# Performance work log

Hardware: AMD Instinct MI355X
Metric: run time of the kernel (lower is better)

Reference implementation:

```python
import jax, jax.numpy as jnp
import numpy as np

WEIGHT_BIT = 8
BIAS_BIT = 32
EPS = 1e-8


def setup_inputs() -> dict:
    key = jax.random.key(0)
    k1, k2, k3, k4 = jax.random.split(key, 4)
    N, IN, OUT = 65536, 512, 512
    # x_q: already-quantized int8-range activations stored as float32
    x_q = jax.random.randint(k1, (N, IN), -128, 128).astype(jnp.float32)
    weight = jax.random.normal(k2, (OUT, IN), dtype=jnp.float32) * 0.05
    bias = jax.random.normal(k3, (OUT,), dtype=jnp.float32) * 0.01
    scale_x = jax.random.uniform(k4, (1,), dtype=jnp.float32, minval=0.01, maxval=0.1)
    return {"x_q": x_q, "weight": weight, "bias": bias, "scale_x": scale_x}


def _symmetric_quant_weight(w, bit):
    # per-output-channel symmetric quantization (min/max over dim=1)
    n = float(2 ** (bit - 1) - 1)  # 127 for 8-bit
    sat = jnp.maximum(jnp.abs(w.min(axis=1)), jnp.abs(w.max(axis=1)))  # [OUT]
    scale = jnp.maximum(sat, EPS) / n                                   # [OUT]
    w_q = jnp.clip(jnp.round(w / scale[:, None]), -n - 1.0, n)
    return w_q, scale


def reference(x_q, weight, bias, scale_x):
    w_q, scale_w = _symmetric_quant_weight(weight, WEIGHT_BIT)
    scale_out = scale_w * scale_x[0]          # [OUT] per-channel output scale
    nb = float(2 ** (BIAS_BIT - 1) - 1)
    b_q = jnp.clip(jnp.round(bias / scale_out), -nb - 1.0, nb)
    # integer-only matmul: int32 GEMM with int32 bias
    out_q = (jnp.dot(x_q.astype(jnp.int32), w_q.astype(jnp.int32).T)
             + b_q.astype(jnp.int32)[None, :])
    return out_q, scale_out.reshape(1, -1)
```

## Files before the change

### kernel.cpp

```cpp
#include <hip/hip_runtime.h>
#include <hip/hip_bf16.h>

typedef __attribute__((ext_vector_type(8))) short bf16x8;
typedef __attribute__((ext_vector_type(4))) float f32x4;

#define KDIM 512
#define NDIM 512
#define BM 128
#define BN 64
#define BK 32
#define NT (KDIM / BK)

__device__ __forceinline__ unsigned int pack_bf16(float a, float b) {
  return (__builtin_bit_cast(unsigned int, a) >> 16) |
         (__builtin_bit_cast(unsigned int, b) & 0xffff0000u);
}

__global__ __launch_bounds__(64)
void quant_w_kernel(const float* __restrict__ W, const float* __restrict__ bias,
                    const float* __restrict__ scale_x,
                    ushort* __restrict__ Wq_arr, float* __restrict__ bq,
                    float* __restrict__ so_out) {
  const int n = blockIdx.x;
  const int l = threadIdx.x;
  const float* row = W + (size_t)n * KDIM;
  float4 v0 = *(const float4*)(row + l * 8);
  float4 v1 = *(const float4*)(row + l * 8 + 4);
  float m = fmaxf(fmaxf(fmaxf(fabsf(v0.x), fabsf(v0.y)), fmaxf(fabsf(v0.z), fabsf(v0.w))),
                  fmaxf(fmaxf(fabsf(v1.x), fabsf(v1.y)), fmaxf(fabsf(v1.z), fabsf(v1.w))));
#pragma unroll
  for (int off = 32; off; off >>= 1) m = fmaxf(m, __shfl_xor(m, off, 64));
  const float scale = fmaxf(m, 1e-8f) / 127.0f;
  float vals[8] = {v0.x, v0.y, v0.z, v0.w, v1.x, v1.y, v1.z, v1.w};
  unsigned int packed[4];
#pragma unroll
  for (int i = 0; i < 4; ++i) {
    float qa = fminf(fmaxf(rintf(vals[2 * i] / scale), -128.f), 127.f);
    float qb = fminf(fmaxf(rintf(vals[2 * i + 1] / scale), -128.f), 127.f);
    packed[i] = pack_bf16(qa, qb);
  }
  const size_t slot = ((size_t)(n >> 4) * 16 + (l >> 2)) * 64 + (n & 15) + (l & 3) * 16;
  *(uint4*)(Wq_arr + slot * 8) = make_uint4(packed[0], packed[1], packed[2], packed[3]);
  if (l == 0) {
    float so = scale * scale_x[0];
    so_out[n] = so;
    bq[n] = rintf(bias[n] / so);
  }
}

__global__ __launch_bounds__(256, 5)
void gemm_kernel(const float* __restrict__ X, const ushort* __restrict__ Wqa,
                 const float* __restrict__ bq, float* __restrict__ Out) {
  __shared__ __align__(16) float As[2][BM * BK];

  const int nblk = gridDim.x;
  int swz = blockIdx.x;
  if ((nblk & 7) == 0)
    swz = (blockIdx.x & 7) * (nblk >> 3) + (blockIdx.x >> 3);
  const int bm = swz >> 3;
  const int bn = swz & 7;

  const int tid = threadIdx.x;
  const int l = tid & 63, w = tid >> 6;
  const int lr = l & 15, lk = l >> 4;

  const float* xbase = X + (size_t)bm * BM * KDIM;
  const ushort* bbase = Wqa + (((size_t)bn * 4 * 16) * 64 + l) * 8;

  f32x4 acc[2][4];
#pragma unroll
  for (int i = 0; i < 2; ++i)
#pragma unroll
    for (int j = 0; j < 4; ++j) acc[i][j] = (f32x4){0.f, 0.f, 0.f, 0.f};

  auto stage = [&](int t, int buf) {
#pragma unroll
    for (int i = 0; i < 4; ++i) {
      int s = i * 256 + tid;
      int row = s >> 3;
      int c = s & 7;
      int sc = c ^ (row & 7);
      const float* g = xbase + (size_t)row * KDIM + t * BK + sc * 4;
      float* lp = &As[buf][0] + (size_t)s * 4;
      __builtin_amdgcn_global_load_lds(
          (const __attribute__((address_space(1))) unsigned int*)g,
          (__attribute__((address_space(3))) unsigned int*)lp, 16, 0, 0);
    }
  };

  auto compute = [&](int t, int buf) {
    const char* pA = (const char*)&As[buf][0];
    bf16x8 bf[4];
#pragma unroll
    for (int nf = 0; nf < 4; ++nf)
      bf[nf] = *(const bf16x8*)(bbase + ((size_t)nf * 16 + t) * 512);
    bf16x8 af[2];
#pragma unroll
    for (int mf = 0; mf < 2; ++mf) {
      int r = w * 32 + mf * 16 + lr;
      int swzr = (r & 7) << 4;
      float4 lo = *(const float4*)(pA + (r * 128 + (((lk * 2) << 4) ^ swzr)));
      float4 hi = *(const float4*)(pA + (r * 128 + (((lk * 2 + 1) << 4) ^ swzr)));
      union { unsigned int u[4]; bf16x8 v; } rr;
      rr.u[0] = pack_bf16(lo.x, lo.y);
      rr.u[1] = pack_bf16(lo.z, lo.w);
      rr.u[2] = pack_bf16(hi.x, hi.y);
      rr.u[3] = pack_bf16(hi.z, hi.w);
      af[mf] = rr.v;
    }
#pragma unroll
    for (int mf = 0; mf < 2; ++mf)
#pragma unroll
      for (int nf = 0; nf < 4; ++nf)
        acc[mf][nf] = __builtin_amdgcn_mfma_f32_16x16x32_bf16(af[mf], bf[nf],
                                                              acc[mf][nf], 0, 0, 0);
  };

  stage(0, 0);
  __syncthreads();
  for (int t = 0; t < NT; ++t) {
    if (t < NT - 1) stage(t + 1, (t + 1) & 1);
    compute(t, t & 1);
    __syncthreads();
  }

  const int colb = bn * BN;
  float bqv[4];
#pragma unroll
  for (int nf = 0; nf < 4; ++nf) bqv[nf] = bq[colb + nf * 16 + lr];
  const int wrow0 = bm * BM + w * 32;
  float* outp = Out + (size_t)(wrow0 + lk * 4) * NDIM + colb + lr;
#pragma unroll
  for (int mf = 0; mf < 2; ++mf)
#pragma unroll
    for (int nf = 0; nf < 4; ++nf)
#pragma unroll
      for (int e = 0; e < 4; ++e)
        outp[(size_t)(mf * 16 + e) * NDIM + nf * 16] = acc[mf][nf][e] + bqv[nf];
}

extern "C" void kernel_launch(void* const* d_in, const int* in_sizes, int n_in,
                              void* d_out, int out_size, void* d_ws, size_t ws_size,
                              hipStream_t stream) {
  const float* x = (const float*)d_in[0];
  const float* weight = (const float*)d_in[1];
  const float* bias = (const float*)d_in[2];
  const float* scale_x = (const float*)d_in[3];
  const int M = in_sizes[0] / KDIM;

  float* out = (float*)d_out;
  float* so_out = out + (size_t)M * NDIM;
  ushort* Wq_arr = (ushort*)d_ws;
  float* bq = (float*)((char*)d_ws + (size_t)NDIM * KDIM * sizeof(ushort));

  quant_w_kernel<<<NDIM, 64, 0, stream>>>(weight, bias, scale_x, Wq_arr, bq, so_out);

  const int blocks = (M / BM) * (NDIM / BN);
  gemm_kernel<<<blocks, 256, 0, stream>>>(x, Wq_arr, bq, out);
}
```

Measured before the change: 327.9 us.

## Stage weight tiles in LDS and deepen GEMM pipeline to four buffers

Weight fragments are now copied into LDS alongside the activation tile with global_load_lds, replacing the direct per-fragment global loads inside the compute step. The main loop is fully unrolled over a 4-buffer ring with prefetch distance 2. Each step waits with explicit vmcnt counts and a single barrier instead of a full __syncthreads per iteration. The larger LDS footprint lowers occupancy, reflected in the launch-bounds hint dropping from 5 to 2 blocks per CU, in exchange for more loads in flight per block.

```diff
diff --git a/kernel.cpp b/kernel.cpp
--- a/kernel.cpp
+++ b/kernel.cpp
@@ -10,6 +10,7 @@
 #define BN 64
 #define BK 32
 #define NT (KDIM / BK)
+#define NBUF 4
 
 __device__ __forceinline__ unsigned int pack_bf16(float a, float b) {
   return (__builtin_bit_cast(unsigned int, a) >> 16) |
@@ -48,10 +49,11 @@
   }
 }
 
-__global__ __launch_bounds__(256, 5)
+__global__ __launch_bounds__(256, 2)
 void gemm_kernel(const float* __restrict__ X, const ushort* __restrict__ Wqa,
                  const float* __restrict__ bq, float* __restrict__ Out) {
-  __shared__ __align__(16) float As[2][BM * BK];
+  __shared__ __align__(16) float As[NBUF][BM * BK];
+  __shared__ __align__(16) ushort Bsh[NBUF][BN * BK];
 
   const int nblk = gridDim.x;
   int swz = blockIdx.x;
@@ -65,7 +67,7 @@
   const int lr = l & 15, lk = l >> 4;
 
   const float* xbase = X + (size_t)bm * BM * KDIM;
-  const ushort* bbase = Wqa + (((size_t)bn * 4 * 16) * 64 + l) * 8;
+  const ushort* wqbase = Wqa + (((size_t)(bn * 4 + w) * 16) * 64 + l) * 8;
 
   f32x4 acc[2][4];
 #pragma unroll
@@ -86,14 +88,22 @@
           (const __attribute__((address_space(1))) unsigned int*)g,
           (__attribute__((address_space(3))) unsigned int*)lp, 16, 0, 0);
     }
+    {
+      const ushort* g = wqbase + (size_t)t * 512;
+      ushort* lp = &Bsh[buf][0] + (size_t)tid * 8;
+      __builtin_amdgcn_global_load_lds(
+          (const __attribute__((address_space(1))) unsigned int*)g,
+          (__attribute__((address_space(3))) unsigned int*)lp, 16, 0, 0);
+    }
   };
 
-  auto compute = [&](int t, int buf) {
+  auto compute = [&](int buf) {
     const char* pA = (const char*)&As[buf][0];
+    const ushort* pB = &Bsh[buf][0];
     bf16x8 bf[4];
 #pragma unroll
     for (int nf = 0; nf < 4; ++nf)
-      bf[nf] = *(const bf16x8*)(bbase + ((size_t)nf * 16 + t) * 512);
+      bf[nf] = *(const bf16x8*)(pB + ((size_t)nf * 64 + l) * 8);
     bf16x8 af[2];
 #pragma unroll
     for (int mf = 0; mf < 2; ++mf) {
@@ -117,12 +127,20 @@
   };
 
   stage(0, 0);
-  __syncthreads();
-  for (int t = 0; t < NT; ++t) {
-    if (t < NT - 1) stage(t + 1, (t + 1) & 1);
-    compute(t, t & 1);
-    __syncthreads();
+  stage(1, 1);
+
+#define STEP(T)                                                                     \
+  {                                                                                 \
+    if ((T) + 2 < NT) stage((T) + 2, ((T) + 2) & 3);                                \
+    asm volatile("s_waitcnt vmcnt(%0)" ::"n"(                                       \
+        ((T) + 2 < NT) ? 10 : (((T) + 1 < NT) ? 5 : 0)) : "memory");                \
+    __builtin_amdgcn_s_barrier();                                                   \
+    compute((T) & 3);                                                               \
+    __builtin_amdgcn_sched_barrier(0);                                              \
   }
+  STEP(0) STEP(1) STEP(2) STEP(3) STEP(4) STEP(5) STEP(6) STEP(7)
+  STEP(8) STEP(9) STEP(10) STEP(11) STEP(12) STEP(13) STEP(14) STEP(15)
+#undef STEP
 
   const int colb = bn * BN;
   float bqv[4];
```

After: 323.6 us. About the same (-1.3%).
